# Kernel tuning notes

Measured on AMD Instinct MI355X. Metric: run time of the kernel, lower is better.

## Reference

```python
import jax, jax.numpy as jnp
import numpy as np

EMBED_DIM = 768
NUM_HEADS = 12
HEAD_DIM = EMBED_DIM // NUM_HEADS
BS, SEQ = 2, 2048
NEG_BIG = -1e20  # matches torch masked_fill value


def setup_inputs() -> dict:
    key = jax.random.key(0)
    ks = jax.random.split(key, 8)
    Q = jax.random.normal(ks[0], (BS, SEQ, EMBED_DIM), dtype=jnp.float32)
    K = jax.random.normal(ks[1], (BS, SEQ, EMBED_DIM), dtype=jnp.float32)
    V = jax.random.normal(ks[2], (BS, SEQ, EMBED_DIM), dtype=jnp.float32)
    mask = jax.random.randint(ks[3], (1, 1, SEQ, SEQ), 0, 2, dtype=jnp.int32)
    scale = 1.0 / np.sqrt(EMBED_DIM).astype(np.float32)
    Wq = jax.random.normal(ks[4], (EMBED_DIM, EMBED_DIM), dtype=jnp.float32) * 0.02
    Wk = jax.random.normal(ks[5], (EMBED_DIM, EMBED_DIM), dtype=jnp.float32) * 0.02
    Wv = jax.random.normal(ks[6], (EMBED_DIM, EMBED_DIM), dtype=jnp.float32) * 0.02
    Wo = jax.random.normal(ks[7], (EMBED_DIM, EMBED_DIM), dtype=jnp.float32) * 0.02
    return {"Q": Q, "K": K, "V": V, "mask": mask,
            "Wq": Wq, "Wk": Wk, "Wv": Wv, "Wo": Wo}


def reference(Q, K, V, mask, Wq, Wk, Wv, Wo):
    bs, q_len, D = Q.shape
    H, hd = NUM_HEADS, HEAD_DIM
    # QKV projections (nn.Linear, no bias): x @ W.T
    q = (Q @ Wq.T).reshape(bs, q_len, H, hd)            # nqhd
    k = (K @ Wk.T).reshape(bs, K.shape[1], H, hd)       # nkhd
    v = (V @ Wv.T).reshape(bs, V.shape[1], H, hd)       # nlhd
    # unfused attention, faithful to source (scale by sqrt(embed_dim)!)
    energy = jnp.einsum('nqhd,nkhd->nhqk', q, k)
    energy = jnp.where(mask == 0, jnp.float32(NEG_BIG), energy)
    attn = jax.nn.softmax(energy * (1.0 / jnp.sqrt(jnp.float32(D))), axis=3)
    out = jnp.einsum('nhql,nlhd->nqhd', attn, v).reshape(bs, q_len, H * hd)
    return out @ Wo.T
```

## Files before the change

### kernel.cpp

```cpp
#include <hip/hip_runtime.h>
#include <cmath>

typedef __bf16 bf16x8 __attribute__((ext_vector_type(8)));
typedef float f32x4 __attribute__((ext_vector_type(4)));
typedef unsigned int u32x4 __attribute__((ext_vector_type(4)));

#define SEQ 2048
#define EMBED 768
#define NHEAD 12
#define HDIM 64
#define NTOK 4096
#define NBH 24
#define NSPLIT 4
#define TILES_PER_SPLIT (SEQ / 64 / NSPLIT)
#define SCALE_LOG2 (1.4426950408889634f * 0.036084391824351615f)

__device__ __forceinline__ void gload_lds16(const __bf16* g, __bf16* l) {
  __builtin_amdgcn_global_load_lds(
      (const __attribute__((address_space(1))) void*)g,
      (__attribute__((address_space(3))) void*)l, 16, 0, 0);
}

__device__ __forceinline__ unsigned pack2(float a, float b) {
  unsigned short lo = __builtin_bit_cast(unsigned short, (__bf16)a);
  unsigned short hi = __builtin_bit_cast(unsigned short, (__bf16)b);
  return (unsigned)lo | ((unsigned)hi << 16);
}

__device__ __forceinline__ void phase_barrier() {
  asm volatile("s_waitcnt vmcnt(0)" ::: "memory");
  __builtin_amdgcn_s_barrier();
  __builtin_amdgcn_sched_barrier(0);
}

__global__ __launch_bounds__(256) void cvt_qkv(const float* __restrict__ Q,
                                               const float* __restrict__ K,
                                               const float* __restrict__ V,
                                               __bf16* __restrict__ Qb,
                                               __bf16* __restrict__ Kb,
                                               __bf16* __restrict__ Vb) {
  const float* s = blockIdx.y == 0 ? Q : blockIdx.y == 1 ? K : V;
  __bf16* d = blockIdx.y == 0 ? Qb : blockIdx.y == 1 ? Kb : Vb;
  size_t i = ((size_t)blockIdx.x * 256 + threadIdx.x) * 8;
  float4 a = *(const float4*)(s + i);
  float4 c = *(const float4*)(s + i + 4);
  bf16x8 r;
  r[0] = (__bf16)a.x; r[1] = (__bf16)a.y; r[2] = (__bf16)a.z; r[3] = (__bf16)a.w;
  r[4] = (__bf16)c.x; r[5] = (__bf16)c.y; r[6] = (__bf16)c.z; r[7] = (__bf16)c.w;
  *(bf16x8*)(d + i) = r;
}

__global__ __launch_bounds__(256) void cvt_w(const float* __restrict__ W0,
                                             const float* __restrict__ W1,
                                             const float* __restrict__ W2,
                                             const float* __restrict__ W3,
                                             __bf16* __restrict__ O0,
                                             __bf16* __restrict__ O1,
                                             __bf16* __restrict__ O2,
                                             __bf16* __restrict__ O3) {
  const float* s = blockIdx.y == 0 ? W0 : blockIdx.y == 1 ? W1 : blockIdx.y == 2 ? W2 : W3;
  __bf16* d = blockIdx.y == 0 ? O0 : blockIdx.y == 1 ? O1 : blockIdx.y == 2 ? O2 : O3;
  size_t i = ((size_t)blockIdx.x * 256 + threadIdx.x) * 8;
  float4 a = *(const float4*)(s + i);
  float4 c = *(const float4*)(s + i + 4);
  bf16x8 r;
  r[0] = (__bf16)a.x; r[1] = (__bf16)a.y; r[2] = (__bf16)a.z; r[3] = (__bf16)a.w;
  r[4] = (__bf16)c.x; r[5] = (__bf16)c.y; r[6] = (__bf16)c.z; r[7] = (__bf16)c.w;
  *(bf16x8*)(d + i) = r;
}

__global__ __launch_bounds__(256) void pack_mask_k(const int* __restrict__ mask,
                                                   unsigned long long* __restrict__ bits) {
  int e = blockIdx.x * 256 + threadIdx.x;
  unsigned long long b = __ballot(mask[e] != 0);
  if ((threadIdx.x & 63) == 0) bits[e >> 6] = b;
}

template <int MODE, typename CT>
__device__ __forceinline__ void gemm_body(const __bf16* __restrict__ A,
                                          const __bf16* __restrict__ B,
                                          CT* __restrict__ C, int N, int row0,
                                          int col0, float alpha, __bf16* As,
                                          __bf16* Bs) {
  const int K = EMBED;
  const int NIT = K / 64;
  const int tid = threadIdx.x;
  const int lane = tid & 63;
  const int wave = tid >> 6;
  const int wr = wave >> 1, wc = wave & 1;
  const int l15 = lane & 15, g = lane >> 4;
  f32x4 acc[4][4] = {};

  const int srow = tid >> 3;
  const int scol8 = (tid & 7) ^ (srow & 7);
  const __bf16* aS = A + (size_t)(row0 + srow) * K + scol8 * 8;
  const __bf16* bS = B + (size_t)(col0 + srow) * K + scol8 * 8;
  __bf16* aL = As + wave * 512;
  __bf16* bL = Bs + wave * 512;

  auto stage = [&](int buf, int k0) {
#pragma unroll
    for (int q = 0; q < 4; ++q) {
      gload_lds16(aS + k0 + (size_t)(q * 32) * K, aL + buf * 8192 + q * 2048);
      gload_lds16(bS + k0 + (size_t)(q * 32) * K, bL + buf * 8192 + q * 2048);
    }
  };

  stage(0, 0);
#pragma unroll 2
  for (int it = 0; it < NIT; ++it) {
    const int c = it & 1;
    phase_barrier();
    if (it + 1 < NIT) stage(1 - c, (it + 1) * 64);
    const __bf16* Asc = As + c * 8192;
    const __bf16* Bsc = Bs + c * 8192;
    bf16x8 af[2][4], bfr[2][4];
#pragma unroll
    for (int i = 0; i < 4; ++i) {
      int row = wr * 64 + i * 16 + l15;
#pragma unroll
      for (int kk = 0; kk < 2; ++kk)
        af[kk][i] =
            *(const bf16x8*)(Asc + row * 64 + ((kk * 4 + g) ^ (row & 7)) * 8);
    }
#pragma unroll
    for (int j = 0; j < 4; ++j) {
      int row = wc * 64 + j * 16 + l15;
#pragma unroll
      for (int kk = 0; kk < 2; ++kk)
        bfr[kk][j] =
            *(const bf16x8*)(Bsc + row * 64 + ((kk * 4 + g) ^ (row & 7)) * 8);
    }
    __builtin_amdgcn_s_setprio(1);
#pragma unroll
    for (int kk = 0; kk < 2; ++kk)
#pragma unroll
      for (int i = 0; i < 4; ++i)
#pragma unroll
        for (int j = 0; j < 4; ++j)
          acc[i][j] = __builtin_amdgcn_mfma_f32_16x16x32_bf16(
              af[kk][i], bfr[kk][j], acc[i][j], 0, 0, 0);
    __builtin_amdgcn_s_setprio(0);
  }
#pragma unroll
  for (int i = 0; i < 4; ++i)
#pragma unroll
    for (int j = 0; j < 4; ++j) {
#pragma unroll
      for (int r = 0; r < 4; ++r) {
        float val = alpha * acc[i][j][r];
        int mrow = row0 + wr * 64 + i * 16 + g * 4 + r;
        int ncol = col0 + wc * 64 + j * 16 + l15;
        if (MODE == 0 || MODE == 3) {
          C[(size_t)mrow * N + ncol] = (CT)val;
        } else if (MODE == 1) {
          int tok = mrow, fcol = ncol;
          int h = fcol >> 6, d = fcol & 63;
          int bh = (tok >> 11) * NHEAD + h;
          int t = (tok >> 6) & 31, kk = tok & 63;
          size_t idx = ((size_t)bh * 32 + t) * 4096 +
                       ((((kk >> 4) * 2 + (d >> 5)) * 64 + ((d >> 3) & 3) * 16 +
                         (kk & 15)) *
                            8 +
                        (d & 7));
          C[idx] = (CT)val;
        } else {
          int fr = mrow, tok = ncol;
          int h = fr >> 6, d = fr & 63;
          int dt = d >> 4, l15c = d & 15;
          int bh = (tok >> 11) * NHEAD + h;
          int t = (tok >> 6) & 31, kk = tok & 63;
          int pc = (kk & 32) | ((kk & 12) << 1) | ((kk & 16) >> 2) | (kk & 3);
          int ks = pc >> 5, Gb = (pc >> 3) & 3, e = pc & 7;
          size_t idx = ((size_t)bh * 32 + t) * 4096 +
                       (((ks * 4 + dt) * 64 + Gb * 16 + l15c) * 8 + e);
          C[idx] = (CT)val;
        }
      }
    }
}

__global__ __launch_bounds__(256) void gemm_qkv(
    const __bf16* __restrict__ Qb, const __bf16* __restrict__ Kb,
    const __bf16* __restrict__ Vb, const __bf16* __restrict__ Wqb,
    const __bf16* __restrict__ Wkb, const __bf16* __restrict__ Wvb,
    __bf16* __restrict__ qh, __bf16* __restrict__ khF, __bf16* __restrict__ vTF) {
  __shared__ __align__(16) __bf16 As[2 * 128 * 64];
  __shared__ __align__(16) __bf16 Bs[2 * 128 * 64];
  if (blockIdx.z == 0)
    gemm_body<0, __bf16>(Qb, Wqb, qh, EMBED, blockIdx.x * 128,
                         blockIdx.y * 128, SCALE_LOG2, As, Bs);
  else if (blockIdx.z == 1)
    gemm_body<1, __bf16>(Kb, Wkb, khF, 0, blockIdx.x * 128, blockIdx.y * 128,
                         1.f, As, Bs);
  else
    gemm_body<2, __bf16>(Wvb, Vb, vTF, 0, blockIdx.y * 128, blockIdx.x * 128,
                         1.f, As, Bs);
}

__global__ __launch_bounds__(256) void gemm_out(const __bf16* __restrict__ AO,
                                                const __bf16* __restrict__ Wob,
                                                float* __restrict__ out) {
  __shared__ __align__(16) __bf16 As[2 * 128 * 64];
  __shared__ __align__(16) __bf16 Bs[2 * 128 * 64];
  gemm_body<3, float>(AO, Wob, out, EMBED, blockIdx.x * 128, blockIdx.y * 128,
                      1.f, As, Bs);
}

__global__ __launch_bounds__(256, 4) void flash_attn(
    const __bf16* __restrict__ qh, const __bf16* __restrict__ khF,
    const __bf16* __restrict__ vTF, const unsigned long long* __restrict__ mbits,
    float* __restrict__ Opart, float* __restrict__ lpart) {
  __shared__ __align__(16) __bf16 Ks[2][4096];
  __shared__ __align__(16) __bf16 Vs[2][4096];
  int lin = blockIdx.x + 16 * (blockIdx.y + NBH * blockIdx.z);
  int wid = (lin & 7) * 192 + (lin >> 3);
  int qb = wid & 15;
  int rest = wid >> 4;
  int bh = rest % NBH;
  int z = rest / NBH;

  const int tid = threadIdx.x;
  const int lane = tid & 63, w = tid >> 6;
  const int l15 = lane & 15, G = lane >> 4;
  const int b = bh / NHEAD, h = bh % NHEAD;
  const int qrow0 = qb * 128 + w * 32;

  bf16x8 qf[2][2];
#pragma unroll
  for (int qg = 0; qg < 2; ++qg) {
    const __bf16* qptr =
        qh + ((size_t)b * SEQ + qrow0 + qg * 16 + l15) * EMBED + h * HDIM + G * 8;
    qf[qg][0] = *(const bf16x8*)qptr;
    qf[qg][1] = *(const bf16x8*)(qptr + 32);
  }
  const u32x4 onesr = {0x3F803F80u, 0x3F803F80u, 0x3F803F80u, 0x3F803F80u};
  const bf16x8 ones = __builtin_bit_cast(bf16x8, onesr);

  f32x4 o[2][4] = {};
  f32x4 ol[2] = {};

  const __bf16* ktile =
      khF + ((size_t)bh * 32 + z * TILES_PER_SPLIT) * 4096 + tid * 8;
  const __bf16* vtile =
      vTF + ((size_t)bh * 32 + z * TILES_PER_SPLIT) * 4096 + tid * 8;
  const unsigned long long* mrow0 =
      mbits + (size_t)(qrow0 + l15) * 32 + z * TILES_PER_SPLIT;
  const unsigned long long* mrow1 = mrow0 + 16 * 32;

  gload_lds16(ktile, &Ks[0][0] + w * 512);
  gload_lds16(ktile + 2048, &Ks[0][0] + w * 512 + 2048);
  gload_lds16(vtile, &Vs[0][0] + w * 512);
  gload_lds16(vtile + 2048, &Vs[0][0] + w * 512 + 2048);
  unsigned long long mb0 = mrow0[0], mb1 = mrow1[0];

#pragma unroll 2
  for (int tt = 0; tt < TILES_PER_SPLIT; ++tt) {
    const int c = tt & 1;
    phase_barrier();
    unsigned long long nmb0 = 0, nmb1 = 0;
    if (tt + 1 < TILES_PER_SPLIT) {
      const __bf16* kt = ktile + (size_t)(tt + 1) * 4096;
      const __bf16* vt = vtile + (size_t)(tt + 1) * 4096;
      __bf16* kd = &Ks[1 - c][0] + w * 512;
      __bf16* vd = &Vs[1 - c][0] + w * 512;
      gload_lds16(kt, kd);
      gload_lds16(kt + 2048, kd + 2048);
      gload_lds16(vt, vd);
      gload_lds16(vt + 2048, vd + 2048);
      nmb0 = mrow0[tt + 1];
      nmb1 = mrow1[tt + 1];
    }

    f32x4 s[2][4];
    __builtin_amdgcn_s_setprio(1);
#pragma unroll
    for (int jj = 0; jj < 4; ++jj) {
      bf16x8 kf0 = *(const bf16x8*)(&Ks[c][0] + (jj * 2 + 0) * 512 + lane * 8);
      bf16x8 kf1 = *(const bf16x8*)(&Ks[c][0] + (jj * 2 + 1) * 512 + lane * 8);
#pragma unroll
      for (int qg = 0; qg < 2; ++qg) {
        f32x4 zz = {};
        zz = __builtin_amdgcn_mfma_f32_16x16x32_bf16(kf0, qf[qg][0], zz, 0, 0, 0);
        zz = __builtin_amdgcn_mfma_f32_16x16x32_bf16(kf1, qf[qg][1], zz, 0, 0, 0);
        s[qg][jj] = zz;
      }
    }
    __builtin_amdgcn_s_setprio(0);

    unsigned pfw[2][2][4];
#pragma unroll
    for (int qg = 0; qg < 2; ++qg) {
      unsigned long long mb = qg == 0 ? mb0 : mb1;
      unsigned mlo = ((unsigned)mb) >> (G * 4);
      unsigned mhi = ((unsigned)(mb >> 32)) >> (G * 4);
#pragma unroll
      for (int jj = 0; jj < 4; ++jj) {
        unsigned bits = (jj < 2 ? mlo : mhi) >> ((jj & 1) * 16);
#pragma unroll
        for (int r = 0; r < 4; ++r) {
          float p = __builtin_amdgcn_exp2f(s[qg][jj][r]);
          int sm = ((int)(bits << (31 - r))) >> 31;
          s[qg][jj][r] = __builtin_bit_cast(
              float, __builtin_bit_cast(unsigned, p) & (unsigned)sm);
        }
      }
#pragma unroll
      for (int ks = 0; ks < 2; ++ks) {
        pfw[qg][ks][0] = pack2(s[qg][2 * ks][0], s[qg][2 * ks][1]);
        pfw[qg][ks][1] = pack2(s[qg][2 * ks][2], s[qg][2 * ks][3]);
        pfw[qg][ks][2] = pack2(s[qg][2 * ks + 1][0], s[qg][2 * ks + 1][1]);
        pfw[qg][ks][3] = pack2(s[qg][2 * ks + 1][2], s[qg][2 * ks + 1][3]);
      }
    }
    __builtin_amdgcn_s_setprio(1);
#pragma unroll
    for (int ks = 0; ks < 2; ++ks) {
      u32x4 p0 = {pfw[0][ks][0], pfw[0][ks][1], pfw[0][ks][2], pfw[0][ks][3]};
      u32x4 p1 = {pfw[1][ks][0], pfw[1][ks][1], pfw[1][ks][2], pfw[1][ks][3]};
      bf16x8 pf0 = __builtin_bit_cast(bf16x8, p0);
      bf16x8 pf1 = __builtin_bit_cast(bf16x8, p1);
      ol[0] = __builtin_amdgcn_mfma_f32_16x16x32_bf16(ones, pf0, ol[0], 0, 0, 0);
      ol[1] = __builtin_amdgcn_mfma_f32_16x16x32_bf16(ones, pf1, ol[1], 0, 0, 0);
#pragma unroll
      for (int dt = 0; dt < 4; ++dt) {
        bf16x8 vf = *(const bf16x8*)(&Vs[c][0] + (ks * 4 + dt) * 512 + lane * 8);
        o[0][dt] = __builtin_amdgcn_mfma_f32_16x16x32_bf16(vf, pf0, o[0][dt], 0, 0, 0);
        o[1][dt] = __builtin_amdgcn_mfma_f32_16x16x32_bf16(vf, pf1, o[1][dt], 0, 0, 0);
      }
    }
    __builtin_amdgcn_s_setprio(0);
    mb0 = nmb0;
    mb1 = nmb1;
  }
#pragma unroll
  for (int qg = 0; qg < 2; ++qg) {
    int qrow = qrow0 + qg * 16 + l15;
    size_t obase = (((size_t)z * NBH + bh) * SEQ + qrow) * HDIM;
    f32x4* op = (f32x4*)(Opart + obase);
#pragma unroll
    for (int dt = 0; dt < 4; ++dt) op[dt * 4 + G] = o[qg][dt];
    if (G == 0)
      lpart[((size_t)z * NBH + bh) * SEQ + qrow] = ol[qg][0];
  }
}

__global__ __launch_bounds__(256) void combine(const float* __restrict__ Opart,
                                               const float* __restrict__ lpart,
                                               __bf16* __restrict__ AO) {
  int idx = blockIdx.x * 256 + threadIdx.x;
  int bhq = idx >> 4, dq = idx & 15;
  int bh = bhq >> 11, q = bhq & (SEQ - 1);
  const f32x4* Ov = (const f32x4*)Opart;
  float lsum = 0.f;
  float r0 = 0.f, r1 = 0.f, r2 = 0.f, r3 = 0.f;
#pragma unroll
  for (int s = 0; s < NSPLIT; ++s) {
    lsum += lpart[(size_t)s * NBH * SEQ + bhq];
    f32x4 a = Ov[(size_t)s * NBH * SEQ * 16 + (size_t)bhq * 16 + dq];
    r0 += a[0];
    r1 += a[1];
    r2 += a[2];
    r3 += a[3];
  }
  float inv = 1.f / lsum;
  int bb = bh / NHEAD, hh = bh % NHEAD;
  unsigned* dst =
      (unsigned*)(AO + ((size_t)bb * SEQ + q) * EMBED + hh * HDIM + dq * 4);
  dst[0] = pack2(r0 * inv, r1 * inv);
  dst[1] = pack2(r2 * inv, r3 * inv);
}

extern "C" void kernel_launch(void* const* d_in, const int* in_sizes, int n_in,
                              void* d_out, int out_size, void* d_ws,
                              size_t ws_size, hipStream_t stream) {
  const float* Q = (const float*)d_in[0];
  const float* K = (const float*)d_in[1];
  const float* V = (const float*)d_in[2];
  const int* mask = (const int*)d_in[3];
  const float* Wq = (const float*)d_in[4];
  const float* Wk = (const float*)d_in[5];
  const float* Wv = (const float*)d_in[6];
  const float* Wo = (const float*)d_in[7];
  float* out = (float*)d_out;

  char* ws = (char*)d_ws;
  const size_t ACT = (size_t)NTOK * EMBED * 2;
  const size_t WMT = (size_t)EMBED * EMBED * 2;
  const size_t OPART_B = (size_t)NSPLIT * NBH * SEQ * HDIM * 4;

  float* Opart = (float*)ws;
  __bf16* Qb = (__bf16*)ws;
  __bf16* Kb = (__bf16*)(ws + ACT);
  __bf16* Vb = (__bf16*)(ws + 2 * ACT);
  __bf16* Wqb = (__bf16*)(ws + 3 * ACT);
  __bf16* Wkb = (__bf16*)(ws + 3 * ACT + WMT);
  __bf16* Wvb = (__bf16*)(ws + 3 * ACT + 2 * WMT);
  size_t off = OPART_B;
  auto alloc = [&](size_t bytes) {
    char* p = ws + off;
    off += (bytes + 255) & ~(size_t)255;
    return p;
  };
  __bf16* Wob = (__bf16*)alloc(WMT);
  __bf16* qh = (__bf16*)alloc(ACT);
  __bf16* khF = (__bf16*)alloc(ACT);
  __bf16* vTF = (__bf16*)alloc(ACT);
  __bf16* AO = (__bf16*)alloc(ACT);
  unsigned long long* mbits =
      (unsigned long long*)alloc((size_t)SEQ * (SEQ / 64) * 8);
  float* lpart = (float*)alloc((size_t)NSPLIT * NBH * SEQ * 4);

  cvt_qkv<<<dim3(NTOK * EMBED / 2048, 3), 256, 0, stream>>>(Q, K, V, Qb, Kb, Vb);
  cvt_w<<<dim3(EMBED * EMBED / 2048, 4), 256, 0, stream>>>(Wq, Wk, Wv, Wo, Wqb,
                                                           Wkb, Wvb, Wob);
  pack_mask_k<<<dim3(SEQ * SEQ / 256), 256, 0, stream>>>(mask, mbits);
  gemm_qkv<<<dim3(NTOK / 128, EMBED / 128, 3), 256, 0, stream>>>(
      Qb, Kb, Vb, Wqb, Wkb, Wvb, qh, khF, vTF);
  flash_attn<<<dim3(SEQ / 128, NBH, NSPLIT), 256, 0, stream>>>(qh, khF, vTF,
                                                               mbits, Opart,
                                                               lpart);
  combine<<<dim3(NBH * SEQ * 16 / 256), 256, 0, stream>>>(Opart, lpart, AO);
  gemm_out<<<dim3(NTOK / 128, EMBED / 128), 256, 0, stream>>>(AO, Wob, out);
  (void)in_sizes; (void)n_in; (void)out_size; (void)ws_size;
}
```

Before: 121.8 us.

## Load K/V fragments directly from global memory instead of staging in LDS

The flash attention kernel stops double-buffering K and V tiles in shared memory via global_load_lds and barriers. Each wave now reads its K/V MFMA fragments straight from global memory (L2/L1 cached), with no LDS, no barriers and no setprio hints. This removes the barrier synchronisation and the LDS footprint, which could raise occupancy. The cost is four waves redundantly fetching the same tiles through the cache with no explicit prefetch overlap, so load latency is exposed.

```diff
diff --git a/kernel.cpp b/kernel.cpp
--- a/kernel.cpp
+++ b/kernel.cpp
@@ -211,8 +211,6 @@
     const __bf16* __restrict__ qh, const __bf16* __restrict__ khF,
     const __bf16* __restrict__ vTF, const unsigned long long* __restrict__ mbits,
     float* __restrict__ Opart, float* __restrict__ lpart) {
-  __shared__ __align__(16) __bf16 Ks[2][4096];
-  __shared__ __align__(16) __bf16 Vs[2][4096];
   int lin = blockIdx.x + 16 * (blockIdx.y + NBH * blockIdx.z);
   int wid = (lin & 7) * 192 + (lin >> 3);
   int qb = wid & 15;
@@ -240,44 +238,25 @@
   f32x4 o[2][4] = {};
   f32x4 ol[2] = {};
 
-  const __bf16* ktile =
-      khF + ((size_t)bh * 32 + z * TILES_PER_SPLIT) * 4096 + tid * 8;
-  const __bf16* vtile =
-      vTF + ((size_t)bh * 32 + z * TILES_PER_SPLIT) * 4096 + tid * 8;
+  const __bf16* kb =
+      khF + ((size_t)bh * 32 + z * TILES_PER_SPLIT) * 4096 + lane * 8;
+  const __bf16* vb =
+      vTF + ((size_t)bh * 32 + z * TILES_PER_SPLIT) * 4096 + lane * 8;
   const unsigned long long* mrow0 =
       mbits + (size_t)(qrow0 + l15) * 32 + z * TILES_PER_SPLIT;
   const unsigned long long* mrow1 = mrow0 + 16 * 32;
 
-  gload_lds16(ktile, &Ks[0][0] + w * 512);
-  gload_lds16(ktile + 2048, &Ks[0][0] + w * 512 + 2048);
-  gload_lds16(vtile, &Vs[0][0] + w * 512);
-  gload_lds16(vtile + 2048, &Vs[0][0] + w * 512 + 2048);
-  unsigned long long mb0 = mrow0[0], mb1 = mrow1[0];
-
 #pragma unroll 2
   for (int tt = 0; tt < TILES_PER_SPLIT; ++tt) {
-    const int c = tt & 1;
-    phase_barrier();
-    unsigned long long nmb0 = 0, nmb1 = 0;
-    if (tt + 1 < TILES_PER_SPLIT) {
-      const __bf16* kt = ktile + (size_t)(tt + 1) * 4096;
-      const __bf16* vt = vtile + (size_t)(tt + 1) * 4096;
-      __bf16* kd = &Ks[1 - c][0] + w * 512;
-      __bf16* vd = &Vs[1 - c][0] + w * 512;
-      gload_lds16(kt, kd);
-      gload_lds16(kt + 2048, kd + 2048);
-      gload_lds16(vt, vd);
-      gload_lds16(vt + 2048, vd + 2048);
-      nmb0 = mrow0[tt + 1];
-      nmb1 = mrow1[tt + 1];
-    }
+    const __bf16* kt = kb + (size_t)tt * 4096;
+    const __bf16* vt = vb + (size_t)tt * 4096;
+    unsigned long long mb0 = mrow0[tt], mb1 = mrow1[tt];
 
     f32x4 s[2][4];
-    __builtin_amdgcn_s_setprio(1);
 #pragma unroll
     for (int jj = 0; jj < 4; ++jj) {
-      bf16x8 kf0 = *(const bf16x8*)(&Ks[c][0] + (jj * 2 + 0) * 512 + lane * 8);
-      bf16x8 kf1 = *(const bf16x8*)(&Ks[c][0] + (jj * 2 + 1) * 512 + lane * 8);
+      bf16x8 kf0 = *(const bf16x8*)(kt + (jj * 2 + 0) * 512);
+      bf16x8 kf1 = *(const bf16x8*)(kt + (jj * 2 + 1) * 512);
 #pragma unroll
       for (int qg = 0; qg < 2; ++qg) {
         f32x4 zz = {};
@@ -286,7 +265,6 @@
         s[qg][jj] = zz;
       }
     }
-    __builtin_amdgcn_s_setprio(0);
 
     unsigned pfw[2][2][4];
 #pragma unroll
@@ -313,7 +291,6 @@
         pfw[qg][ks][3] = pack2(s[qg][2 * ks + 1][2], s[qg][2 * ks + 1][3]);
       }
     }
-    __builtin_amdgcn_s_setprio(1);
 #pragma unroll
     for (int ks = 0; ks < 2; ++ks) {
       u32x4 p0 = {pfw[0][ks][0], pfw[0][ks][1], pfw[0][ks][2], pfw[0][ks][3]};
@@ -324,14 +301,11 @@
       ol[1] = __builtin_amdgcn_mfma_f32_16x16x32_bf16(ones, pf1, ol[1], 0, 0, 0);
 #pragma unroll
       for (int dt = 0; dt < 4; ++dt) {
-        bf16x8 vf = *(const bf16x8*)(&Vs[c][0] + (ks * 4 + dt) * 512 + lane * 8);
+        bf16x8 vf = *(const bf16x8*)(vt + (ks * 4 + dt) * 512);
         o[0][dt] = __builtin_amdgcn_mfma_f32_16x16x32_bf16(vf, pf0, o[0][dt], 0, 0, 0);
         o[1][dt] = __builtin_amdgcn_mfma_f32_16x16x32_bf16(vf, pf1, o[1][dt], 0, 0, 0);
       }
     }
-    __builtin_amdgcn_s_setprio(0);
-    mb0 = nmb0;
-    mb1 = nmb1;
   }
 #pragma unroll
   for (int qg = 0; qg < 2; ++qg) {
```

Measured after the change: 140.4 us. 1.15x slower.
